# Kernel optimization log

Hardware: AMD Instinct MI355X
Metric: run time of the kernel (lower is better)

Reference implementation:

```python
import jax, jax.numpy as jnp
import numpy as np

K = 3
K2 = K * K
EPS = 1e-5


def conv2d(x, w, stride=1, pad=1):
    return jax.lax.conv_general_dilated(
        x, w, (stride, stride), [(pad, pad), (pad, pad)],
        dimension_numbers=("NCHW", "OIHW", "NCHW"))


def bilinear_sample(x, py, px):
    """x: [B,C,H,W]; py,px: [B,Ho,Wo,K2] float sample coords.
    Zero padding outside bounds (torchvision deform_conv2d semantics).
    Returns [B,C,Ho,Wo,K2]."""
    B, C, H, W = x.shape
    Ho, Wo = py.shape[1], py.shape[2]
    y0 = jnp.floor(py)
    x0 = jnp.floor(px)
    wy1 = py - y0
    wx1 = px - x0
    x_flat = x.reshape(B, C, H * W)

    def gather(yi, xi):
        valid = (yi >= 0) & (yi < H) & (xi >= 0) & (xi < W)
        yc = jnp.clip(yi, 0, H - 1).astype(jnp.int32)
        xc = jnp.clip(xi, 0, W - 1).astype(jnp.int32)
        idx = (yc * W + xc).reshape(B, 1, -1)          # [B,1,N]
        v = jnp.take_along_axis(x_flat, idx, axis=2)   # [B,C,N]
        return v * valid.reshape(B, 1, -1).astype(x.dtype)

    w00 = ((1 - wy1) * (1 - wx1)).reshape(B, 1, -1)
    w01 = ((1 - wy1) * wx1).reshape(B, 1, -1)
    w10 = (wy1 * (1 - wx1)).reshape(B, 1, -1)
    w11 = (wy1 * wx1).reshape(B, 1, -1)
    val = (w00 * gather(y0, x0) + w01 * gather(y0, x0 + 1)
           + w10 * gather(y0 + 1, x0) + w11 * gather(y0 + 1, x0 + 1))
    return val.reshape(B, C, Ho, Wo, K2)


def deform_conv_bn_relu(x, d, offset_w, conv_w, gamma, beta):
    # offset branch: 3x3 conv on d, clamp to [-1,1]
    offset = jnp.clip(conv2d(d, offset_w, 1, 1), -1.0, 1.0)  # [B,2*K2,H,W]
    B, Cin, H, W = x.shape
    Cout = conv_w.shape[0]
    off = offset.reshape(B, K2, 2, H, W)
    dy = off[:, :, 0].transpose(0, 2, 3, 1)  # [B,H,W,K2]
    dx = off[:, :, 1].transpose(0, 2, 3, 1)
    kh = (jnp.arange(K2) // K).astype(jnp.float32)
    kw = (jnp.arange(K2) % K).astype(jnp.float32)
    # sample coords: out pixel + kernel tap - padding + learned offset
    py = (jnp.arange(H, dtype=jnp.float32)[None, :, None, None] - 1.0
          + kh[None, None, None, :] + dy)
    px = (jnp.arange(W, dtype=jnp.float32)[None, None, :, None] - 1.0
          + kw[None, None, None, :] + dx)
    sampled = bilinear_sample(x, py, px)  # [B,Cin,H,W,K2]
    out = jnp.einsum('bchwk,ock->bohw', sampled,
                     conv_w.reshape(Cout, Cin, K2))
    # BatchNorm2d (training forward: biased batch stats) + ReLU
    mean = out.mean(axis=(0, 2, 3))
    var = out.var(axis=(0, 2, 3))
    inv = gamma / jnp.sqrt(var + EPS)
    out = (out - mean[None, :, None, None]) * inv[None, :, None, None] \
        + beta[None, :, None, None]
    out = jax.nn.relu(out)
    return out, offset


def setup_inputs() -> dict:
    key = jax.random.key(0)
    k1, k2, k3, k4 = jax.random.split(key, 4)
    B, C, H, W = 4, 64, 160, 160
    Cout, offC = 64, 64
    x = jax.random.normal(k1, (B, C, H, W), dtype=jnp.float32)
    d = jax.random.normal(k2, (B, offC, H, W), dtype=jnp.float32)
    # torch zero-inits offset_conv; use small random weights so the
    # bilinear gather path is actually exercised with fractional offsets
    offset_w = jax.random.normal(k3, (2 * K2, offC, K, K), dtype=jnp.float32) * 0.01
    conv_w = jax.random.normal(k4, (Cout, C, K, K), dtype=jnp.float32) * (1.0 / np.sqrt(C * K2))
    gamma = jnp.ones((Cout,), dtype=jnp.float32)
    beta = jnp.zeros((Cout,), dtype=jnp.float32)
    return {"x": x, "d": d, "offset_w": offset_w, "conv_w": conv_w,
            "gamma": gamma, "beta": beta}


def reference(x, d, offset_w, conv_w, gamma, beta):
    return deform_conv_bn_relu(x, d, offset_w, conv_w, gamma, beta)
```

## Files before the change

kernel.cpp:

```cpp
#include <hip/hip_runtime.h>
#include <hip/hip_bf16.h>

#define BB 4
#define HH 160
#define WW 160
#define HWD (HH * WW)
#define OUT_ELEMS (BB * 64 * HWD)
#define OFF_ELEMS (BB * 18 * HWD)
#define EPSBN 1e-5f
#define CHSTRIDE (8 * HWD)
#define NSLOT 256

typedef __attribute__((ext_vector_type(8))) _Float16 f16x8;
typedef __attribute__((ext_vector_type(4))) float f32x4;

__device__ inline unsigned short f16bits(float a) {
  _Float16 h = (_Float16)a;
  unsigned short u;
  __builtin_memcpy(&u, &h, 2);
  return u;
}

__device__ inline unsigned pkrtz(float a, float b) {
  __fp16 __attribute__((ext_vector_type(2))) t =
      __builtin_amdgcn_cvt_pkrtz(a, b);
  unsigned u;
  __builtin_memcpy(&u, &t, 4);
  return u;
}

__device__ inline f16x8 load8cvt(const float* pp) {
  union { f16x8 v; unsigned u[4]; } r;
  r.u[0] = pkrtz(pp[0], pp[HWD]);
  r.u[1] = pkrtz(pp[2 * HWD], pp[3 * HWD]);
  r.u[2] = pkrtz(pp[4 * HWD], pp[5 * HWD]);
  r.u[3] = pkrtz(pp[6 * HWD], pp[7 * HWD]);
  return r.v;
}

__device__ inline void ldsbar() {
  asm volatile("s_waitcnt lgkmcnt(0)" ::: "memory");
  __builtin_amdgcn_s_barrier();
}

__device__ inline void tile_map(int blk, int& b, int& ty0, int& tx0) {
  int t = (blk & 7) * 200 + (blk >> 3);
  b = t / 400;
  int r = t % 400;
  ty0 = (r / 10) * 4;
  tx0 = (r % 10) * 16;
}

__global__ void prep_kernel(const float* __restrict__ cw,
                            const float* __restrict__ ow,
                            unsigned short* __restrict__ Bp,
                            unsigned short* __restrict__ B2p,
                            float* __restrict__ part) {
  int i = blockIdx.x * 256 + threadIdx.x;
  if (i < 32768) part[i] = 0.f;
  if (i < 49152) {
    int j = i & 7, l = (i >> 3) & 63, rest = i >> 9;
    int ki = rest % 24, nt = rest / 24;
    int kp = ki * 32 + ((l >> 4) << 3) + j;
    int chunk = kp / 96, kq = kp % 96;
    int t = kq >> 3, c = kq & 7;
    int n = nt * 16 + (l & 15);
    float v = (t < 9) ? cw[n * 576 + (chunk * 8 + c) * 9 + t] : 0.f;
    Bp[i] = f16bits(v);
  }
  if (i < 24576) {
    int j = i & 7, l = (i >> 3) & 63, rest = i >> 9;
    int ki = rest % 24, nt = rest / 24;
    int kp = ki * 32 + ((l >> 4) << 3) + j;
    int chunk = kp / 96, kq = kp % 96;
    int t = kq >> 3, c = kq & 7;
    int n = nt * 16 + (l & 15);
    float v = (t < 9 && n < 18) ? ow[n * 576 + (chunk * 8 + c) * 9 + t] : 0.f;
    B2p[i] = f16bits(v);
  }
}

__global__ __launch_bounds__(256, 4) void fused_kernel(
    const float* __restrict__ x, const float* __restrict__ d,
    const f16x8* __restrict__ Bp, const f16x8* __restrict__ B2p,
    float* __restrict__ out, float* __restrict__ off_out,
    float* __restrict__ part) {
  int b, ty0, tx0;
  tile_map(blockIdx.x, b, ty0, tx0);
  const int tid = threadIdx.x;
  const int wv = tid >> 6, lane = tid & 63;
  const int lo = lane >> 4, li = lane & 15;
  const int px = li, py = wv;
  const int h = ty0 + py, w = tx0 + px;

  __shared__ __align__(16) _Float16 patch[189 * 8];
  __shared__ f16x8 Af[768];
  __shared__ float offs_s[64 * 18];

  const f16x8 zero8 = {(_Float16)0, (_Float16)0, (_Float16)0, (_Float16)0,
                       (_Float16)0, (_Float16)0, (_Float16)0, (_Float16)0};

  int goff2 = 0, laddr2 = 0;
  bool inr2 = tid < 189, ok2 = false;
  {
    int p = tid;
    int r = p / 21, col = p % 21;
    int gy = ty0 - 2 + r, gx = tx0 - 2 + col;
    ok2 = inr2 && gy >= 0 && gy < HH && gx >= 0 && gx < WW;
    goff2 = ((b * 64) * HH + gy) * WW + gx;
    laddr2 = p * 8;
  }

  f32x4 acc0{0.f, 0.f, 0.f, 0.f}, acc1{0.f, 0.f, 0.f, 0.f};
  const int ntA = wv >> 1, mh = wv & 1;
  {
    int poff[3];
    bool tre[3];
#pragma unroll
    for (int kk = 0; kk < 3; ++kk) {
      int t = kk * 4 + lo;
      tre[kk] = (t < 9);
      poff[kk] = tre[kk] ? ((py + t / 3) * 18 + px + t % 3) : 0;
    }

    int goff1 = 0, laddr1 = 0;
    bool inr1 = tid < 108, ok1 = false;
    {
      int p = tid;
      int r = p / 18, col = p % 18;
      int gy = ty0 - 1 + r, gx = tx0 - 1 + col;
      ok1 = inr1 && gy >= 0 && gy < HH && gx >= 0 && gx < WW;
      goff1 = ((b * 64) * HH + gy) * WW + gx;
      laddr1 = p * 8;
    }
    f16x8 g1 = zero8;
    if (ok1) g1 = load8cvt(d + goff1);

    for (int chunk = 0; chunk < 8; ++chunk) {
      f16x8 bw0 = B2p[((ntA * 24 + chunk * 3 + 0) << 6) + lane];
      f16x8 bw1 = B2p[((ntA * 24 + chunk * 3 + 1) << 6) + lane];
      f16x8 bw2 = B2p[((ntA * 24 + chunk * 3 + 2) << 6) + lane];
      if (inr1) *(f16x8*)&patch[laddr1] = g1;
      ldsbar();
      int nco = ((chunk < 7) ? (chunk + 1) : 7) * CHSTRIDE;
      if (ok1) g1 = load8cvt(d + goff1 + nco);
#pragma unroll
      for (int kk = 0; kk < 3; ++kk) {
        f16x8 av = tre[kk] ? *(const f16x8*)(patch + poff[kk] * 8) : zero8;
        Af[((wv * 3 + kk) << 6) + lane] = av;
      }
      ldsbar();
#pragma unroll
      for (int kk = 0; kk < 3; ++kk) {
        f16x8 bw = (kk == 0) ? bw0 : (kk == 1) ? bw1 : bw2;
        acc0 = __builtin_amdgcn_mfma_f32_16x16x32_f16(
            Af[(((mh * 2) * 3 + kk) << 6) + lane], bw, acc0, 0, 0, 0);
        acc1 = __builtin_amdgcn_mfma_f32_16x16x32_f16(
            Af[(((mh * 2 + 1) * 3 + kk) << 6) + lane], bw, acc1, 0, 0, 0);
      }
    }
  }

  f16x8 gv = zero8;
  if (ok2) gv = load8cvt(x + goff2);

  {
    const int n = ntA * 16 + li;
    if (n < 18) {
#pragma unroll
      for (int f = 0; f < 2; ++f) {
        int mf = mh * 2 + f;
        f32x4 a = f ? acc1 : acc0;
        float* po =
            off_out + ((b * 18 + n) * HH + ty0 + mf) * WW + tx0 + lo * 4;
        float4 v;
        v.x = fminf(1.f, fmaxf(-1.f, a[0]));
        v.y = fminf(1.f, fmaxf(-1.f, a[1]));
        v.z = fminf(1.f, fmaxf(-1.f, a[2]));
        v.w = fminf(1.f, fmaxf(-1.f, a[3]));
        *(float4*)po = v;
        int pix = mf * 16 + lo * 4;
        offs_s[(pix + 0) * 18 + n] = v.x;
        offs_s[(pix + 1) * 18 + n] = v.y;
        offs_s[(pix + 2) * 18 + n] = v.z;
        offs_s[(pix + 3) * 18 + n] = v.w;
      }
    }
  }
  ldsbar();

  int bs[3];
  float W00[3], W01[3], W10[3], W11[3];
  bool tre[3];
#pragma unroll
  for (int kk = 0; kk < 3; ++kk) {
    int t = kk * 4 + lo;
    tre[kk] = (t < 9);
    if (tre[kk]) {
      float dy = offs_s[(py * 16 + px) * 18 + 2 * t];
      float dx = offs_s[(py * 16 + px) * 18 + 2 * t + 1];
      float pyf = (float)(h - 1 + t / 3) + dy;
      float pxf = (float)(w - 1 + t % 3) + dx;
      float y0 = floorf(pyf), x0 = floorf(pxf);
      float wy = pyf - y0, wx = pxf - x0;
      bs[kk] = ((int)y0 - (ty0 - 2)) * 21 + ((int)x0 - (tx0 - 2));
      W00[kk] = (1.f - wy) * (1.f - wx);
      W01[kk] = (1.f - wy) * wx;
      W10[kk] = wy * (1.f - wx);
      W11[kk] = wy * wx;
    } else {
      bs[kk] = 0;
      W00[kk] = W01[kk] = W10[kk] = W11[kk] = 0.f;
    }
  }

  f32x4 acc[4];
#pragma unroll
  for (int i = 0; i < 4; ++i) acc[i] = f32x4{0.f, 0.f, 0.f, 0.f};
  const int nt = wv;

  for (int chunk = 0; chunk < 8; ++chunk) {
    f16x8 bw0 = Bp[((nt * 24 + chunk * 3 + 0) << 6) + lane];
    f16x8 bw1 = Bp[((nt * 24 + chunk * 3 + 1) << 6) + lane];
    f16x8 bw2 = Bp[((nt * 24 + chunk * 3 + 2) << 6) + lane];
    if (inr2) *(f16x8*)&patch[laddr2] = gv;
    ldsbar();
    int nco = ((chunk < 7) ? (chunk + 1) : 7) * CHSTRIDE;
    if (ok2) gv = load8cvt(x + goff2 + nco);
#pragma unroll
    for (int kk = 0; kk < 3; ++kk) {
      f16x8 av;
      if (tre[kk]) {
        const _Float16* q = patch + bs[kk] * 8;
        f16x8 p00 = *(const f16x8*)(q);
        f16x8 p01 = *(const f16x8*)(q + 8);
        f16x8 p10 = *(const f16x8*)(q + 168);
        f16x8 p11 = *(const f16x8*)(q + 176);
        _Float16 w0 = (_Float16)W00[kk], w1 = (_Float16)W01[kk];
        _Float16 w2 = (_Float16)W10[kk], w3 = (_Float16)W11[kk];
        f16x8 w0v = {w0, w0, w0, w0, w0, w0, w0, w0};
        f16x8 w1v = {w1, w1, w1, w1, w1, w1, w1, w1};
        f16x8 w2v = {w2, w2, w2, w2, w2, w2, w2, w2};
        f16x8 w3v = {w3, w3, w3, w3, w3, w3, w3, w3};
        av = p00 * w0v + p01 * w1v + p10 * w2v + p11 * w3v;
      } else {
        av = zero8;
      }
      Af[((wv * 3 + kk) << 6) + lane] = av;
    }
    ldsbar();
#pragma unroll
    for (int kk = 0; kk < 3; ++kk) {
      f16x8 bw = (kk == 0) ? bw0 : (kk == 1) ? bw1 : bw2;
#pragma unroll
      for (int mf = 0; mf < 4; ++mf)
        acc[mf] = __builtin_amdgcn_mfma_f32_16x16x32_f16(
            Af[((mf * 3 + kk) << 6) + lane], bw, acc[mf], 0, 0, 0);
    }
  }
  const int n = nt * 16 + li;
  float s = 0.f, s2 = 0.f;
#pragma unroll
  for (int mf = 0; mf < 4; ++mf) {
    float* po = out + ((b * 64 + n) * HH + ty0 + mf) * WW + tx0 + lo * 4;
    *(float4*)po = make_float4(acc[mf][0], acc[mf][1], acc[mf][2], acc[mf][3]);
#pragma unroll
    for (int r = 0; r < 4; ++r) {
      float v = acc[mf][r];
      s += v;
      s2 = fmaf(v, v, s2);
    }
  }
  s += __shfl_xor(s, 16);  s += __shfl_xor(s, 32);
  s2 += __shfl_xor(s2, 16); s2 += __shfl_xor(s2, 32);
  if (lo == 0) {
    int slot = blockIdx.x & (NSLOT - 1);
    atomicAdd(&part[n * NSLOT + slot], s);
    atomicAdd(&part[(64 + n) * NSLOT + slot], s2);
  }
}

__global__ __launch_bounds__(256) void reduce_kernel(
    const float* __restrict__ part, double* __restrict__ sums) {
  const int j = blockIdx.x;
  __shared__ double sh[256];
  sh[threadIdx.x] = (double)part[j * NSLOT + threadIdx.x];
  __syncthreads();
  for (int t = 128; t > 0; t >>= 1) {
    if (threadIdx.x < t) sh[threadIdx.x] += sh[threadIdx.x + t];
    __syncthreads();
  }
  if (threadIdx.x == 0) sums[j] = sh[0];
}

__global__ __launch_bounds__(256) void bnapply_kernel(
    float* __restrict__ out, const double* __restrict__ sums,
    const float* __restrict__ gamma, const float* __restrict__ beta) {
  const int i = blockIdx.x * 256 + threadIdx.x;
  if (i >= OUT_ELEMS / 4) return;
  const int o = (i / (HWD / 4)) & 63;
  const float n_inv = 1.0f / (float)(BB * HWD);
  float mean = (float)sums[o] * n_inv;
  float var = (float)sums[64 + o] * n_inv - mean * mean;
  float inv = gamma[o] * rsqrtf(var + EPSBN);
  float bt = beta[o];
  float4 v = ((float4*)out)[i];
  v.x = fmaxf(0.f, (v.x - mean) * inv + bt);
  v.y = fmaxf(0.f, (v.y - mean) * inv + bt);
  v.z = fmaxf(0.f, (v.z - mean) * inv + bt);
  v.w = fmaxf(0.f, (v.w - mean) * inv + bt);
  ((float4*)out)[i] = v;
}

extern "C" void kernel_launch(void* const* d_in, const int* in_sizes, int n_in,
                              void* d_out, int out_size, void* d_ws, size_t ws_size,
                              hipStream_t stream) {
  const float* x = (const float*)d_in[0];
  const float* d = (const float*)d_in[1];
  const float* ow = (const float*)d_in[2];
  const float* cw = (const float*)d_in[3];
  const float* gamma = (const float*)d_in[4];
  const float* beta = (const float*)d_in[5];

  float* out = (float*)d_out;
  float* off_out = out + OUT_ELEMS;

  double* sums = (double*)d_ws;
  unsigned short* Bp = (unsigned short*)((char*)d_ws + 1024);
  unsigned short* B2p = Bp + 49152;
  float* part = (float*)(B2p + 24576);

  prep_kernel<<<192, 256, 0, stream>>>(cw, ow, Bp, B2p, part);

  fused_kernel<<<1600, 256, 0, stream>>>(x, d, (const f16x8*)Bp,
                                         (const f16x8*)B2p, out, off_out,
                                         part);

  reduce_kernel<<<128, 256, 0, stream>>>(part, sums);
  bnapply_kernel<<<(OUT_ELEMS / 4 + 255) / 256, 256, 0, stream>>>(
      out, sums, gamma, beta);
}
```

Before: 154.3 us.

## Double-buffer LDS patch and A tiles to halve barriers per chunk

Adds double buffers for the LDS patch and A-fragment arrays in both the offset conv loop and the deformable sampling loop. Each chunk now needs one barrier instead of two: the next chunk's patch is written into the alternate buffer while the current one is consumed, and the global prefetch runs two chunks ahead. This targets barrier stalls and should overlap LDS staging with MFMA work, at the cost of roughly doubling the LDS footprint, which may reduce occupancy below the launch bound of 4 blocks.

```diff
diff --git a/kernel.cpp b/kernel.cpp
--- a/kernel.cpp
+++ b/kernel.cpp
@@ -93,8 +93,8 @@
   const int px = li, py = wv;
   const int h = ty0 + py, w = tx0 + px;
 
-  __shared__ __align__(16) _Float16 patch[189 * 8];
-  __shared__ f16x8 Af[768];
+  __shared__ __align__(16) _Float16 patch[2][189 * 8];
+  __shared__ f16x8 Af[2][768];
   __shared__ float offs_s[64 * 18];
 
   const f16x8 zero8 = {(_Float16)0, (_Float16)0, (_Float16)0, (_Float16)0,
@@ -135,28 +135,32 @@
     }
     f16x8 g1 = zero8;
     if (ok1) g1 = load8cvt(d + goff1);
+    if (inr1) *(f16x8*)&patch[0][laddr1] = g1;
+    ldsbar();
+    if (ok1) g1 = load8cvt(d + goff1 + CHSTRIDE);
 
     for (int chunk = 0; chunk < 8; ++chunk) {
+      const int cur = chunk & 1, nxt = cur ^ 1;
       f16x8 bw0 = B2p[((ntA * 24 + chunk * 3 + 0) << 6) + lane];
       f16x8 bw1 = B2p[((ntA * 24 + chunk * 3 + 1) << 6) + lane];
       f16x8 bw2 = B2p[((ntA * 24 + chunk * 3 + 2) << 6) + lane];
-      if (inr1) *(f16x8*)&patch[laddr1] = g1;
+#pragma unroll
+      for (int kk = 0; kk < 3; ++kk) {
+        f16x8 av =
+            tre[kk] ? *(const f16x8*)(patch[cur] + poff[kk] * 8) : zero8;
+        Af[cur][((wv * 3 + kk) << 6) + lane] = av;
+      }
+      if (chunk < 7 && inr1) *(f16x8*)&patch[nxt][laddr1] = g1;
       ldsbar();
-      int nco = ((chunk < 7) ? (chunk + 1) : 7) * CHSTRIDE;
-      if (ok1) g1 = load8cvt(d + goff1 + nco);
-#pragma unroll
-      for (int kk = 0; kk < 3; ++kk) {
-        f16x8 av = tre[kk] ? *(const f16x8*)(patch + poff[kk] * 8) : zero8;
-        Af[((wv * 3 + kk) << 6) + lane] = av;
-      }
-      ldsbar();
+      if (chunk < 6 && ok1)
+        g1 = load8cvt(d + goff1 + (chunk + 2) * CHSTRIDE);
 #pragma unroll
       for (int kk = 0; kk < 3; ++kk) {
         f16x8 bw = (kk == 0) ? bw0 : (kk == 1) ? bw1 : bw2;
         acc0 = __builtin_amdgcn_mfma_f32_16x16x32_f16(
-            Af[(((mh * 2) * 3 + kk) << 6) + lane], bw, acc0, 0, 0, 0);
+            Af[cur][(((mh * 2) * 3 + kk) << 6) + lane], bw, acc0, 0, 0, 0);
         acc1 = __builtin_amdgcn_mfma_f32_16x16x32_f16(
-            Af[(((mh * 2 + 1) * 3 + kk) << 6) + lane], bw, acc1, 0, 0, 0);
+            Af[cur][(((mh * 2 + 1) * 3 + kk) << 6) + lane], bw, acc1, 0, 0, 0);
       }
     }
   }
@@ -187,6 +191,7 @@
       }
     }
   }
+  if (inr2) *(f16x8*)&patch[0][laddr2] = gv;
   ldsbar();
 
   int bs[3];
@@ -219,19 +224,18 @@
   for (int i = 0; i < 4; ++i) acc[i] = f32x4{0.f, 0.f, 0.f, 0.f};
   const int nt = wv;
 
+  if (ok2) gv = load8cvt(x + goff2 + CHSTRIDE);
+
   for (int chunk = 0; chunk < 8; ++chunk) {
+    const int cur = chunk & 1, nxt = cur ^ 1;
     f16x8 bw0 = Bp[((nt * 24 + chunk * 3 + 0) << 6) + lane];
     f16x8 bw1 = Bp[((nt * 24 + chunk * 3 + 1) << 6) + lane];
     f16x8 bw2 = Bp[((nt * 24 + chunk * 3 + 2) << 6) + lane];
-    if (inr2) *(f16x8*)&patch[laddr2] = gv;
-    ldsbar();
-    int nco = ((chunk < 7) ? (chunk + 1) : 7) * CHSTRIDE;
-    if (ok2) gv = load8cvt(x + goff2 + nco);
 #pragma unroll
     for (int kk = 0; kk < 3; ++kk) {
       f16x8 av;
       if (tre[kk]) {
-        const _Float16* q = patch + bs[kk] * 8;
+        const _Float16* q = patch[cur] + bs[kk] * 8;
         f16x8 p00 = *(const f16x8*)(q);
         f16x8 p01 = *(const f16x8*)(q + 8);
         f16x8 p10 = *(const f16x8*)(q + 168);
@@ -246,16 +250,19 @@
       } else {
         av = zero8;
       }
-      Af[((wv * 3 + kk) << 6) + lane] = av;
-    }
+      Af[cur][((wv * 3 + kk) << 6) + lane] = av;
+    }
+    if (chunk < 7 && inr2) *(f16x8*)&patch[nxt][laddr2] = gv;
     ldsbar();
+    if (chunk < 6 && ok2)
+      gv = load8cvt(x + goff2 + (chunk + 2) * CHSTRIDE);
 #pragma unroll
     for (int kk = 0; kk < 3; ++kk) {
       f16x8 bw = (kk == 0) ? bw0 : (kk == 1) ? bw1 : bw2;
 #pragma unroll
       for (int mf = 0; mf < 4; ++mf)
         acc[mf] = __builtin_amdgcn_mfma_f32_16x16x32_f16(
-            Af[((mf * 3 + kk) << 6) + lane], bw, acc[mf], 0, 0, 0);
+            Af[cur][((mf * 3 + kk) << 6) + lane], bw, acc[mf], 0, 0, 0);
     }
   }
   const int n = nt * 16 + li;
```

After: 152.6 us, median of 2. Within noise of the previous version (-1.1%).
